# Optimization experiments

Measured on AMD Instinct MI355X. Metric: run time of the kernel, lower is better.

Reference implementation:

```python
import jax, jax.numpy as jnp
import numpy as np

N_NODES = 50000
N_EDGES = 800000
IN_CH = 96
HID = 128
OUT_CH = 2


def _glorot(key, shape):
    lim = 1.0 / np.sqrt(shape[0])
    return jax.random.uniform(key, shape, jnp.float32, -lim, lim)


def setup_inputs() -> dict:
    key = jax.random.key(0)
    ks = jax.random.split(key, 16)
    x = jax.random.normal(ks[0], (N_NODES, IN_CH), jnp.float32)
    edge_index = jax.random.randint(ks[1], (2, N_EDGES), 0, N_NODES, jnp.int64)
    dims = [(IN_CH, HID), (HID, HID), (HID, HID // 2)]
    params = {}
    for i, (di, do) in enumerate(dims, start=1):
        params[f"Wl{i}"] = _glorot(ks[2 * i], (di, do))      # neighbor (lin_l)
        params[f"Wr{i}"] = _glorot(ks[2 * i + 1], (di, do))  # root (lin_r)
        params[f"b{i}"] = jnp.zeros((do,), jnp.float32)
    params["Wc"] = _glorot(ks[10], (HID // 2, OUT_CH))
    params["bc"] = jnp.zeros((OUT_CH,), jnp.float32)
    return {"x": x, "edge_index": edge_index, **params}


def _sage_conv(x, src, dst, Wl, Wr, b):
    # scatter-mean of source-node features into destination nodes (PyG mean aggr)
    n = x.shape[0]
    agg = jax.ops.segment_sum(x[src], dst, num_segments=n)          # [N, d]
    cnt = jax.ops.segment_sum(jnp.ones((src.shape[0], 1), x.dtype), dst, num_segments=n)
    mean = agg / jnp.maximum(cnt, 1.0)
    return mean @ Wl + x @ Wr + b


def reference(x, edge_index, Wl1, Wr1, b1, Wl2, Wr2, b2, Wl3, Wr3, b3, Wc, bc):
    src, dst = edge_index[0], edge_index[1]
    h = jax.nn.relu(_sage_conv(x, src, dst, Wl1, Wr1, b1))
    h = jax.nn.relu(_sage_conv(h, src, dst, Wl2, Wr2, b2))
    h = jax.nn.relu(_sage_conv(h, src, dst, Wl3, Wr3, b3))
    return h @ Wc + bc  # [N, 2] logits (dropout is identity at inference)
```

## Files before the change

### kernel.cpp

```cpp
#include <hip/hip_runtime.h>

#define N_NODES 50000
#define N_EDGES 800000
#define SCAN_NB ((N_NODES + 255) / 256)

#define NB_E 128
#define CH (N_EDGES / NB_E)
#define RSZ 25000
#define HALF_WORDS (RSZ / 2)

#define CVT_ITEMS  (N_NODES * 96 / 4)
#define CVT_NB  ((CVT_ITEMS + 255) / 256)
#define PACK1_NB 12
#define PACK2_NB 16
#define PACK3_NB 8
#define PREP_NB (CVT_NB + PACK1_NB + PACK2_NB + PACK3_NB)

typedef __attribute__((ext_vector_type(8))) short short8;
typedef __attribute__((ext_vector_type(8))) unsigned short ushort8;
typedef __attribute__((ext_vector_type(4))) float f32x4;

__device__ __forceinline__ float bf2f(unsigned short u) {
  unsigned int x = ((unsigned int)u) << 16;
  return __builtin_bit_cast(float, x);
}
__device__ __forceinline__ unsigned short f2bf(float f) {
  unsigned int x = __builtin_bit_cast(unsigned int, f);
  unsigned int r = x + 0x7FFFu + ((x >> 16) & 1u);
  return (unsigned short)(r >> 16);
}


__device__ __forceinline__ void pack_w_section(const float* __restrict__ Wl,
                                               const float* __restrict__ Wr,
                                               ushort* __restrict__ wcat,
                                               int K, int J2, int bid) {
  int idx = bid * 256 + threadIdx.x;
  int Jcat = 2 * J2;
  int total = (K / 8) * Jcat;
  if (idx >= total) return;
  int kk8 = idx / Jcat, j = idx % Jcat;
  const float* W = (j < J2) ? Wl : Wr;
  int jj = (j < J2) ? j : j - J2;
  ushort8 v;
  #pragma unroll
  for (int i = 0; i < 8; i++) v[i] = f2bf(W[(kk8 * 8 + i) * J2 + jj]);
  *(ushort8*)(wcat + (size_t)idx * 8) = v;
}

__global__ __launch_bounds__(256) void prep_kernel(
    const float* __restrict__ x, ushort* __restrict__ xb,
    const float* __restrict__ Wl1, const float* __restrict__ Wr1, ushort* __restrict__ wcat1,
    const float* __restrict__ Wl2, const float* __restrict__ Wr2, ushort* __restrict__ wcat2,
    const float* __restrict__ Wl3, const float* __restrict__ Wr3, ushort* __restrict__ wcat3) {
  int bid = blockIdx.x;
  if (bid < CVT_NB) {
    int i = bid * 256 + threadIdx.x;
    if (i < CVT_ITEMS) {
      f32x4 v = __builtin_nontemporal_load((const f32x4*)(x + i * 4));
      ushort4 o = make_ushort4(f2bf(v.x), f2bf(v.y), f2bf(v.z), f2bf(v.w));
      *(ushort4*)(xb + i * 4) = o;
    }
    return;
  }
  bid -= CVT_NB;
  if (bid < PACK1_NB) { pack_w_section(Wl1, Wr1, wcat1, 96, 128, bid); return; }
  bid -= PACK1_NB;
  if (bid < PACK2_NB) { pack_w_section(Wl2, Wr2, wcat2, 128, 128, bid); return; }
  bid -= PACK2_NB;
  pack_w_section(Wl3, Wr3, wcat3, 128, 64, bid);
}


__global__ __launch_bounds__(256) void hist_lds(const int* __restrict__ dst,
                                                ushort* __restrict__ hist_g) {
  __shared__ unsigned hist[HALF_WORDS];
  for (int j = threadIdx.x; j < HALF_WORDS; j += 256) hist[j] = 0;
  __syncthreads();
  int b = blockIdx.x >> 1, r = blockIdx.x & 1;
  int base = b * CH;
  for (int i = threadIdx.x; i < CH; i += 256) {
    int d = __builtin_nontemporal_load(dst + base + i);
    unsigned ld = (unsigned)(d - r * RSZ);
    if (ld < RSZ) atomicAdd(&hist[ld >> 1], (ld & 1) ? 65536u : 1u);
  }
  __syncthreads();
  unsigned* outp = (unsigned*)(hist_g + (size_t)b * N_NODES + r * RSZ);
  for (int j = threadIdx.x; j < HALF_WORDS; j += 256) outp[j] = hist[j];
}

__device__ __forceinline__ int block_excl_scan_256(int v, int tid, int* tot_out) {
  __shared__ int ws[4];
  int lane = tid & 63, wid = tid >> 6;
  int incl = v;
  #pragma unroll
  for (int off = 1; off < 64; off <<= 1) {
    int t = __shfl_up(incl, off);
    if (lane >= off) incl += t;
  }
  if (lane == 63) ws[wid] = incl;
  __syncthreads();
  int woff = 0;
  #pragma unroll
  for (int w = 0; w < 4; w++) woff += (w < wid) ? ws[w] : 0;
  *tot_out = ws[0] + ws[1] + ws[2] + ws[3];
  return woff + incl - v;
}

__global__ __launch_bounds__(256) void scanA(const ushort* __restrict__ hist_g,
                                             ushort* __restrict__ cum_g,
                                             int* __restrict__ rowptr,
                                             int* __restrict__ blocksum, int n) {
  int i = blockIdx.x * 256 + threadIdx.x;
  int run = 0;
  if (i < n) {
    for (int b = 0; b < NB_E; b++) {
      size_t o = (size_t)b * N_NODES + i;
      int c = hist_g[o];
      cum_g[o] = (ushort)run;
      run += c;
    }
  }
  int tot;
  int excl = block_excl_scan_256(run, threadIdx.x, &tot);
  if (i < n) rowptr[i] = excl;
  if (threadIdx.x == 0) blocksum[blockIdx.x] = tot;
}

__global__ __launch_bounds__(256) void scanBC(const int* __restrict__ blocksum,
                                              int* __restrict__ rowptr, int n) {
  __shared__ int exls[256];
  int tid = threadIdx.x;
  int v = (tid < SCAN_NB) ? blocksum[tid] : 0;
  int tot;
  int excl = block_excl_scan_256(v, tid, &tot);
  exls[tid] = excl;
  __syncthreads();
  int myoff = exls[blockIdx.x];
  int i = blockIdx.x * 256 + tid;
  if (i < n) rowptr[i] += myoff;
  if (blockIdx.x == 0 && tid == 0) rowptr[n] = tot;
}

__global__ __launch_bounds__(256) void fill_lds(const int* __restrict__ src,
                                                const int* __restrict__ dst,
                                                const ushort* __restrict__ cum_g,
                                                const int* __restrict__ rowptr,
                                                ushort* __restrict__ csr) {
  __shared__ unsigned cur[HALF_WORDS];
  int b = blockIdx.x >> 1, r = blockIdx.x & 1;
  const unsigned* cg = (const unsigned*)(cum_g + (size_t)b * N_NODES + r * RSZ);
  for (int j = threadIdx.x; j < HALF_WORDS; j += 256) cur[j] = cg[j];
  __syncthreads();
  int base = b * CH;
  for (int i = threadIdx.x; i < CH; i += 256) {
    int d = __builtin_nontemporal_load(dst + base + i);
    int s = __builtin_nontemporal_load(src + base + i);
    unsigned ld = (unsigned)(d - r * RSZ);
    if (ld < RSZ) {
      unsigned old = atomicAdd(&cur[ld >> 1], (ld & 1) ? 65536u : 1u);
      unsigned loc = (ld & 1) ? (old >> 16) : (old & 0xffffu);
      csr[(size_t)rowptr[d] + loc] = (ushort)s;
    }
  }
}

template <int K, int J2>
__global__ __launch_bounds__(256) void gemm_mfma(
    const ushort* __restrict__ hb, const ushort* __restrict__ wcat,
    ushort* __restrict__ tl, ushort* __restrict__ tr, int n) {
  constexpr int Jcat = 2 * J2;
  constexpr int NT = Jcat / 16;
  constexpr int KS = K / 32;

  int tid = threadIdx.x;
  int wid = tid >> 6, lane = tid & 63;
  int rg = lane >> 4, lc = lane & 15;
  int row0 = blockIdx.x * 128;
  int r0 = row0 + wid * 32 + lc;
  int r1 = r0 + 16;
  long ar0 = (long)min(r0, n - 1) * K;
  long ar1 = (long)min(r1, n - 1) * K;

  f32x4 acc[2][NT];
  #pragma unroll
  for (int mt = 0; mt < 2; mt++)
    #pragma unroll
    for (int jt = 0; jt < NT; jt++) acc[mt][jt] = (f32x4){0.f, 0.f, 0.f, 0.f};

  #pragma unroll
  for (int ks = 0; ks < KS; ks++) {
    int koff = ks * 32 + rg * 8;
    short8 a0 = *(const short8*)(hb + ar0 + koff);
    short8 a1 = *(const short8*)(hb + ar1 + koff);
    int kk8 = ks * 4 + rg;
    #pragma unroll
    for (int jt = 0; jt < NT; jt++) {
      short8 bfr = *(const short8*)(wcat + ((size_t)kk8 * Jcat + jt * 16 + lc) * 8);
      acc[0][jt] = __builtin_amdgcn_mfma_f32_16x16x32_bf16(a0, bfr, acc[0][jt], 0, 0, 0);
      acc[1][jt] = __builtin_amdgcn_mfma_f32_16x16x32_bf16(a1, bfr, acc[1][jt], 0, 0, 0);
    }
  }

  #pragma unroll
  for (int mt = 0; mt < 2; mt++) {
    int rbase = wid * 32 + mt * 16 + rg * 4;
    #pragma unroll
    for (int jt = 0; jt < NT; jt++) {
      int col = jt * 16 + lc;
      ushort* outp = (col < J2) ? tl : tr;
      int cm = (col < J2) ? col : col - J2;
      #pragma unroll
      for (int r = 0; r < 4; r++) {
        int grow = row0 + rbase + r;
        if (grow < n) outp[(size_t)grow * J2 + cm] = f2bf(acc[mt][jt][r]);
      }
    }
  }
}

__global__ __launch_bounds__(256) void agg_relu128(
    const ushort* __restrict__ tl, const ushort* __restrict__ tr,
    const float* __restrict__ bias,
    const int* __restrict__ rowptr, const ushort* __restrict__ csr,
    ushort* __restrict__ hout, int n) {
  int node = blockIdx.x * 16 + (threadIdx.x >> 4);
  int lane = threadIdx.x & 15;
  if (node >= n) return;
  int lo = rowptr[node], hi = rowptr[node + 1];
  const ushort* tb = tl + lane * 8;

  float s[8];
  #pragma unroll
  for (int i = 0; i < 8; i++) s[i] = 0.f;

  int e = lo;
  for (; e + 7 < hi; e += 8) {
    ushort8 v[8];
    #pragma unroll
    for (int q = 0; q < 8; q++) v[q] = *(const ushort8*)(tb + (size_t)csr[e + q] * 128);
    #pragma unroll
    for (int q = 0; q < 8; q++)
      #pragma unroll
      for (int i = 0; i < 8; i++) s[i] += bf2f(v[q][i]);
  }
  for (; e + 1 < hi; e += 2) {
    ushort8 v0 = *(const ushort8*)(tb + (size_t)csr[e] * 128);
    ushort8 v1 = *(const ushort8*)(tb + (size_t)csr[e + 1] * 128);
    #pragma unroll
    for (int i = 0; i < 8; i++) s[i] += bf2f(v0[i]) + bf2f(v1[i]);
  }
  if (e < hi) {
    ushort8 v0 = *(const ushort8*)(tb + (size_t)csr[e] * 128);
    #pragma unroll
    for (int i = 0; i < 8; i++) s[i] += bf2f(v0[i]);
  }

  int deg = hi - lo;
  float inv = (deg > 0) ? 1.f / (float)deg : 0.f;
  ushort8 tv = *(const ushort8*)(tr + (size_t)node * 128 + lane * 8);
  float4 b0 = *(const float4*)(bias + lane * 8);
  float4 b1 = *(const float4*)(bias + lane * 8 + 4);
  float bb[8] = {b0.x, b0.y, b0.z, b0.w, b1.x, b1.y, b1.z, b1.w};
  ushort8 o;
  #pragma unroll
  for (int i = 0; i < 8; i++) {
    float v = s[i] * inv + bf2f(tv[i]) + bb[i];
    o[i] = f2bf(v > 0.f ? v : 0.f);
  }
  *(ushort8*)(hout + (size_t)node * 128 + lane * 8) = o;
}

__global__ __launch_bounds__(256) void agg_head(
    const ushort* __restrict__ tl, const ushort* __restrict__ tr,
    const float* __restrict__ bias, const float* __restrict__ Wc,
    const float* __restrict__ bc,
    const int* __restrict__ rowptr, const ushort* __restrict__ csr,
    float* __restrict__ out, int n) {
  int node = blockIdx.x * 32 + (threadIdx.x >> 3);
  int lane = threadIdx.x & 7;
  if (node >= n) return;
  int lo = rowptr[node], hi = rowptr[node + 1];
  const ushort* tb = tl + lane * 8;

  float s[8];
  #pragma unroll
  for (int i = 0; i < 8; i++) s[i] = 0.f;

  int e = lo;
  for (; e + 7 < hi; e += 8) {
    ushort8 v[8];
    #pragma unroll
    for (int q = 0; q < 8; q++) v[q] = *(const ushort8*)(tb + (size_t)csr[e + q] * 64);
    #pragma unroll
    for (int q = 0; q < 8; q++)
      #pragma unroll
      for (int i = 0; i < 8; i++) s[i] += bf2f(v[q][i]);
  }
  for (; e + 1 < hi; e += 2) {
    ushort8 v0 = *(const ushort8*)(tb + (size_t)csr[e] * 64);
    ushort8 v1 = *(const ushort8*)(tb + (size_t)csr[e + 1] * 64);
    #pragma unroll
    for (int i = 0; i < 8; i++) s[i] += bf2f(v0[i]) + bf2f(v1[i]);
  }
  if (e < hi) {
    ushort8 v0 = *(const ushort8*)(tb + (size_t)csr[e] * 64);
    #pragma unroll
    for (int i = 0; i < 8; i++) s[i] += bf2f(v0[i]);
  }

  int deg = hi - lo;
  float inv = (deg > 0) ? 1.f / (float)deg : 0.f;
  ushort8 tv = *(const ushort8*)(tr + (size_t)node * 64 + lane * 8);
  float p0 = 0.f, p1 = 0.f;
  #pragma unroll
  for (int i = 0; i < 8; i++) {
    int k = lane * 8 + i;
    float v = s[i] * inv + bf2f(tv[i]) + bias[k];
    v = v > 0.f ? v : 0.f;
    p0 += v * Wc[k * 2 + 0];
    p1 += v * Wc[k * 2 + 1];
  }
  #pragma unroll
  for (int off = 1; off < 8; off <<= 1) {
    p0 += __shfl_xor(p0, off);
    p1 += __shfl_xor(p1, off);
  }
  if (lane == 0) {
    out[(size_t)node * 2 + 0] = p0 + bc[0];
    out[(size_t)node * 2 + 1] = p1 + bc[1];
  }
}

extern "C" void kernel_launch(void* const* d_in, const int* in_sizes, int n_in,
                              void* d_out, int out_size, void* d_ws, size_t ws_size,
                              hipStream_t stream) {
  const float* x   = (const float*)d_in[0];
  const int*   ei  = (const int*)d_in[1];
  const float* Wl1 = (const float*)d_in[2];
  const float* Wr1 = (const float*)d_in[3];
  const float* b1  = (const float*)d_in[4];
  const float* Wl2 = (const float*)d_in[5];
  const float* Wr2 = (const float*)d_in[6];
  const float* b2  = (const float*)d_in[7];
  const float* Wl3 = (const float*)d_in[8];
  const float* Wr3 = (const float*)d_in[9];
  const float* b3  = (const float*)d_in[10];
  const float* Wc  = (const float*)d_in[11];
  const float* bc  = (const float*)d_in[12];
  float* out = (float*)d_out;

  const int* src = ei;
  const int* dst = ei + N_EDGES;

  char* ws = (char*)d_ws;
  size_t off = 0;
  auto alloc = [&](size_t bytes) -> void* {
    void* p = ws + off;
    off += (bytes + 255) & ~(size_t)255;
    return p;
  };
  int*    rowptr   = (int*)alloc((N_NODES + 1) * sizeof(int));
  ushort* csr      = (ushort*)alloc(N_EDGES * sizeof(ushort));
  int*    blocksum = (int*)alloc(256 * sizeof(int));
  ushort* xb       = (ushort*)alloc((size_t)N_NODES * 96 * 2);
  ushort* wcat1    = (ushort*)alloc((size_t)96 * 256 * 2);
  ushort* wcat2    = (ushort*)alloc((size_t)128 * 256 * 2);
  ushort* wcat3    = (ushort*)alloc((size_t)128 * 128 * 2);
  ushort* tl       = (ushort*)alloc((size_t)N_NODES * 128 * 2);
  ushort* tr       = (ushort*)alloc((size_t)N_NODES * 128 * 2);
  ushort* hA       = (ushort*)alloc((size_t)N_NODES * 128 * 2);
  ushort* hB       = (ushort*)alloc((size_t)N_NODES * 128 * 2);
  (void)ws_size; (void)n_in; (void)in_sizes; (void)out_size;

  ushort* hist_g = tl;
  ushort* cum_g  = tr;

  prep_kernel<<<PREP_NB, 256, 0, stream>>>(x, xb,
                                           Wl1, Wr1, wcat1,
                                           Wl2, Wr2, wcat2,
                                           Wl3, Wr3, wcat3);

  hist_lds<<<NB_E * 2, 256, 0, stream>>>(dst, hist_g);
  scanA<<<SCAN_NB, 256, 0, stream>>>(hist_g, cum_g, rowptr, blocksum, N_NODES);
  scanBC<<<SCAN_NB, 256, 0, stream>>>(blocksum, rowptr, N_NODES);
  fill_lds<<<NB_E * 2, 256, 0, stream>>>(src, dst, cum_g, rowptr, csr);

  const int gemm_grid = (N_NODES + 127) / 128;
  const int agg_grid  = (N_NODES + 15) / 16;
  const int head_grid = (N_NODES + 31) / 32;

  gemm_mfma<96, 128><<<gemm_grid, 256, 0, stream>>>(xb, wcat1, tl, tr, N_NODES);
  agg_relu128<<<agg_grid, 256, 0, stream>>>(tl, tr, b1, rowptr, csr, hA, N_NODES);
  gemm_mfma<128, 128><<<gemm_grid, 256, 0, stream>>>(hA, wcat2, tl, tr, N_NODES);
  agg_relu128<<<agg_grid, 256, 0, stream>>>(tl, tr, b2, rowptr, csr, hB, N_NODES);
  gemm_mfma<128, 64><<<gemm_grid, 256, 0, stream>>>(hB, wcat3, tl, tr, N_NODES);
  agg_head<<<head_grid, 256, 0, stream>>>(tl, tr, b3, Wc, bc, rowptr, csr, out, N_NODES);
}
```

Before: 198.7 us.

## Fuse histogram into prep kernel and CSR fill with first-layer GEMM

Merges the edge histogram pass into the prep/convert kernel and the CSR fill pass into the first GEMM launch, using block-index ranges to run independent work concurrently and cutting two launches. Histogram and cumulative buffers move to dedicated workspace so they no longer alias tl/tr, which the fused GEMM writes. NB_E is halved to 64, so each histogram block handles twice as many edges while the scan loop gets shorter. Fused blocks carry 50KB of LDS even on the GEMM/convert paths, which may reduce occupancy for those blocks.

```diff
diff --git a/kernel.cpp b/kernel.cpp
--- a/kernel.cpp
+++ b/kernel.cpp
@@ -4,17 +4,21 @@
 #define N_EDGES 800000
 #define SCAN_NB ((N_NODES + 255) / 256)
 
-#define NB_E 128
+#define NB_E 64
 #define CH (N_EDGES / NB_E)
 #define RSZ 25000
 #define HALF_WORDS (RSZ / 2)
+#define CSRB (NB_E * 2)
 
 #define CVT_ITEMS  (N_NODES * 96 / 4)
 #define CVT_NB  ((CVT_ITEMS + 255) / 256)
 #define PACK1_NB 12
 #define PACK2_NB 16
 #define PACK3_NB 8
-#define PREP_NB (CVT_NB + PACK1_NB + PACK2_NB + PACK3_NB)
+#define K1_NB (CSRB + CVT_NB + PACK1_NB + PACK2_NB + PACK3_NB)
+
+#define GEMM_NB ((N_NODES + 127) / 128)
+#define K4_NB (GEMM_NB + CSRB)
 
 typedef __attribute__((ext_vector_type(8))) short short8;
 typedef __attribute__((ext_vector_type(8))) unsigned short ushort8;
@@ -30,6 +34,59 @@
   return (unsigned short)(r >> 16);
 }
 
+template <int K, int J2>
+__device__ __forceinline__ void gemm_body(int bid,
+    const ushort* __restrict__ hb, const ushort* __restrict__ wcat,
+    ushort* __restrict__ tl, ushort* __restrict__ tr, int n) {
+  constexpr int Jcat = 2 * J2;
+  constexpr int NT = Jcat / 16;
+  constexpr int KS = K / 32;
+
+  int tid = threadIdx.x;
+  int wid = tid >> 6, lane = tid & 63;
+  int rg = lane >> 4, lc = lane & 15;
+  int row0 = bid * 128;
+  int r0 = row0 + wid * 32 + lc;
+  int r1 = r0 + 16;
+  long ar0 = (long)min(r0, n - 1) * K;
+  long ar1 = (long)min(r1, n - 1) * K;
+
+  f32x4 acc[2][NT];
+  #pragma unroll
+  for (int mt = 0; mt < 2; mt++)
+    #pragma unroll
+    for (int jt = 0; jt < NT; jt++) acc[mt][jt] = (f32x4){0.f, 0.f, 0.f, 0.f};
+
+  #pragma unroll
+  for (int ks = 0; ks < KS; ks++) {
+    int koff = ks * 32 + rg * 8;
+    short8 a0 = *(const short8*)(hb + ar0 + koff);
+    short8 a1 = *(const short8*)(hb + ar1 + koff);
+    int kk8 = ks * 4 + rg;
+    #pragma unroll
+    for (int jt = 0; jt < NT; jt++) {
+      short8 bfr = *(const short8*)(wcat + ((size_t)kk8 * Jcat + jt * 16 + lc) * 8);
+      acc[0][jt] = __builtin_amdgcn_mfma_f32_16x16x32_bf16(a0, bfr, acc[0][jt], 0, 0, 0);
+      acc[1][jt] = __builtin_amdgcn_mfma_f32_16x16x32_bf16(a1, bfr, acc[1][jt], 0, 0, 0);
+    }
+  }
+
+  #pragma unroll
+  for (int mt = 0; mt < 2; mt++) {
+    int rbase = wid * 32 + mt * 16 + rg * 4;
+    #pragma unroll
+    for (int jt = 0; jt < NT; jt++) {
+      int col = jt * 16 + lc;
+      ushort* outp = (col < J2) ? tl : tr;
+      int cm = (col < J2) ? col : col - J2;
+      #pragma unroll
+      for (int r = 0; r < 4; r++) {
+        int grow = row0 + rbase + r;
+        if (grow < n) outp[(size_t)grow * J2 + cm] = f2bf(acc[mt][jt][r]);
+      }
+    }
+  }
+}
 
 __device__ __forceinline__ void pack_w_section(const float* __restrict__ Wl,
                                                const float* __restrict__ Wr,
@@ -48,12 +105,30 @@
   *(ushort8*)(wcat + (size_t)idx * 8) = v;
 }
 
-__global__ __launch_bounds__(256) void prep_kernel(
+__global__ __launch_bounds__(256) void k1_hist_prep(
+    const int* __restrict__ dst, ushort* __restrict__ hist_g,
     const float* __restrict__ x, ushort* __restrict__ xb,
     const float* __restrict__ Wl1, const float* __restrict__ Wr1, ushort* __restrict__ wcat1,
     const float* __restrict__ Wl2, const float* __restrict__ Wr2, ushort* __restrict__ wcat2,
     const float* __restrict__ Wl3, const float* __restrict__ Wr3, ushort* __restrict__ wcat3) {
+  __shared__ unsigned hist[HALF_WORDS];
   int bid = blockIdx.x;
+  if (bid < CSRB) {
+    for (int j = threadIdx.x; j < HALF_WORDS; j += 256) hist[j] = 0;
+    __syncthreads();
+    int b = bid >> 1, r = bid & 1;
+    int base = b * CH;
+    for (int i = threadIdx.x; i < CH; i += 256) {
+      int d = __builtin_nontemporal_load(dst + base + i);
+      unsigned ld = (unsigned)(d - r * RSZ);
+      if (ld < RSZ) atomicAdd(&hist[ld >> 1], (ld & 1) ? 65536u : 1u);
+    }
+    __syncthreads();
+    unsigned* outp = (unsigned*)(hist_g + (size_t)b * N_NODES + r * RSZ);
+    for (int j = threadIdx.x; j < HALF_WORDS; j += 256) outp[j] = hist[j];
+    return;
+  }
+  bid -= CSRB;
   if (bid < CVT_NB) {
     int i = bid * 256 + threadIdx.x;
     if (i < CVT_ITEMS) {
@@ -71,23 +146,6 @@
   pack_w_section(Wl3, Wr3, wcat3, 128, 64, bid);
 }
 
-
-__global__ __launch_bounds__(256) void hist_lds(const int* __restrict__ dst,
-                                                ushort* __restrict__ hist_g) {
-  __shared__ unsigned hist[HALF_WORDS];
-  for (int j = threadIdx.x; j < HALF_WORDS; j += 256) hist[j] = 0;
-  __syncthreads();
-  int b = blockIdx.x >> 1, r = blockIdx.x & 1;
-  int base = b * CH;
-  for (int i = threadIdx.x; i < CH; i += 256) {
-    int d = __builtin_nontemporal_load(dst + base + i);
-    unsigned ld = (unsigned)(d - r * RSZ);
-    if (ld < RSZ) atomicAdd(&hist[ld >> 1], (ld & 1) ? 65536u : 1u);
-  }
-  __syncthreads();
-  unsigned* outp = (unsigned*)(hist_g + (size_t)b * N_NODES + r * RSZ);
-  for (int j = threadIdx.x; j < HALF_WORDS; j += 256) outp[j] = hist[j];
-}
 
 __device__ __forceinline__ int block_excl_scan_256(int v, int tid, int* tot_out) {
   __shared__ int ws[4];
@@ -114,6 +172,7 @@
   int i = blockIdx.x * 256 + threadIdx.x;
   int run = 0;
   if (i < n) {
+    #pragma unroll 4
     for (int b = 0; b < NB_E; b++) {
       size_t o = (size_t)b * N_NODES + i;
       int c = hist_g[o];
@@ -142,13 +201,20 @@
   if (blockIdx.x == 0 && tid == 0) rowptr[n] = tot;
 }
 
-__global__ __launch_bounds__(256) void fill_lds(const int* __restrict__ src,
-                                                const int* __restrict__ dst,
-                                                const ushort* __restrict__ cum_g,
-                                                const int* __restrict__ rowptr,
-                                                ushort* __restrict__ csr) {
+__global__ __launch_bounds__(256) void k4_gemm1_fill(
+    const ushort* __restrict__ xb, const ushort* __restrict__ wcat1,
+    ushort* __restrict__ tl, ushort* __restrict__ tr,
+    const int* __restrict__ src, const int* __restrict__ dst,
+    const ushort* __restrict__ cum_g, const int* __restrict__ rowptr,
+    ushort* __restrict__ csr, int n) {
   __shared__ unsigned cur[HALF_WORDS];
-  int b = blockIdx.x >> 1, r = blockIdx.x & 1;
+  int bid = blockIdx.x;
+  if (bid < GEMM_NB) {
+    gemm_body<96, 128>(bid, xb, wcat1, tl, tr, n);
+    return;
+  }
+  bid -= GEMM_NB;
+  int b = bid >> 1, r = bid & 1;
   const unsigned* cg = (const unsigned*)(cum_g + (size_t)b * N_NODES + r * RSZ);
   for (int j = threadIdx.x; j < HALF_WORDS; j += 256) cur[j] = cg[j];
   __syncthreads();
@@ -169,54 +235,7 @@
 __global__ __launch_bounds__(256) void gemm_mfma(
     const ushort* __restrict__ hb, const ushort* __restrict__ wcat,
     ushort* __restrict__ tl, ushort* __restrict__ tr, int n) {
-  constexpr int Jcat = 2 * J2;
-  constexpr int NT = Jcat / 16;
-  constexpr int KS = K / 32;
-
-  int tid = threadIdx.x;
-  int wid = tid >> 6, lane = tid & 63;
-  int rg = lane >> 4, lc = lane & 15;
-  int row0 = blockIdx.x * 128;
-  int r0 = row0 + wid * 32 + lc;
-  int r1 = r0 + 16;
-  long ar0 = (long)min(r0, n - 1) * K;
-  long ar1 = (long)min(r1, n - 1) * K;
-
-  f32x4 acc[2][NT];
-  #pragma unroll
-  for (int mt = 0; mt < 2; mt++)
-    #pragma unroll
-    for (int jt = 0; jt < NT; jt++) acc[mt][jt] = (f32x4){0.f, 0.f, 0.f, 0.f};
-
-  #pragma unroll
-  for (int ks = 0; ks < KS; ks++) {
-    int koff = ks * 32 + rg * 8;
-    short8 a0 = *(const short8*)(hb + ar0 + koff);
-    short8 a1 = *(const short8*)(hb + ar1 + koff);
-    int kk8 = ks * 4 + rg;
-    #pragma unroll
-    for (int jt = 0; jt < NT; jt++) {
-      short8 bfr = *(const short8*)(wcat + ((size_t)kk8 * Jcat + jt * 16 + lc) * 8);
-      acc[0][jt] = __builtin_amdgcn_mfma_f32_16x16x32_bf16(a0, bfr, acc[0][jt], 0, 0, 0);
-      acc[1][jt] = __builtin_amdgcn_mfma_f32_16x16x32_bf16(a1, bfr, acc[1][jt], 0, 0, 0);
-    }
-  }
-
-  #pragma unroll
-  for (int mt = 0; mt < 2; mt++) {
-    int rbase = wid * 32 + mt * 16 + rg * 4;
-    #pragma unroll
-    for (int jt = 0; jt < NT; jt++) {
-      int col = jt * 16 + lc;
-      ushort* outp = (col < J2) ? tl : tr;
-      int cm = (col < J2) ? col : col - J2;
-      #pragma unroll
-      for (int r = 0; r < 4; r++) {
-        int grow = row0 + rbase + r;
-        if (grow < n) outp[(size_t)grow * J2 + cm] = f2bf(acc[mt][jt][r]);
-      }
-    }
-  }
+  gemm_body<K, J2>(blockIdx.x, hb, wcat, tl, tr, n);
 }
 
 __global__ __launch_bounds__(256) void agg_relu128(
@@ -363,6 +382,8 @@
   int*    rowptr   = (int*)alloc((N_NODES + 1) * sizeof(int));
   ushort* csr      = (ushort*)alloc(N_EDGES * sizeof(ushort));
   int*    blocksum = (int*)alloc(256 * sizeof(int));
+  ushort* hist_g   = (ushort*)alloc((size_t)NB_E * N_NODES * 2);
+  ushort* cum_g    = (ushort*)alloc((size_t)NB_E * N_NODES * 2);
   ushort* xb       = (ushort*)alloc((size_t)N_NODES * 96 * 2);
   ushort* wcat1    = (ushort*)alloc((size_t)96 * 256 * 2);
   ushort* wcat2    = (ushort*)alloc((size_t)128 * 256 * 2);
@@ -373,27 +394,21 @@
   ushort* hB       = (ushort*)alloc((size_t)N_NODES * 128 * 2);
   (void)ws_size; (void)n_in; (void)in_sizes; (void)out_size;
 
-  ushort* hist_g = tl;
-  ushort* cum_g  = tr;
-
-  prep_kernel<<<PREP_NB, 256, 0, stream>>>(x, xb,
-                                           Wl1, Wr1, wcat1,
-                                           Wl2, Wr2, wcat2,
-                                           Wl3, Wr3, wcat3);
-
-  hist_lds<<<NB_E * 2, 256, 0, stream>>>(dst, hist_g);
+  k1_hist_prep<<<K1_NB, 256, 0, stream>>>(dst, hist_g, x, xb,
+                                          Wl1, Wr1, wcat1,
+                                          Wl2, Wr2, wcat2,
+                                          Wl3, Wr3, wcat3);
   scanA<<<SCAN_NB, 256, 0, stream>>>(hist_g, cum_g, rowptr, blocksum, N_NODES);
   scanBC<<<SCAN_NB, 256, 0, stream>>>(blocksum, rowptr, N_NODES);
-  fill_lds<<<NB_E * 2, 256, 0, stream>>>(src, dst, cum_g, rowptr, csr);
-
-  const int gemm_grid = (N_NODES + 127) / 128;
+  k4_gemm1_fill<<<K4_NB, 256, 0, stream>>>(xb, wcat1, tl, tr,
+                                           src, dst, cum_g, rowptr, csr, N_NODES);
+
   const int agg_grid  = (N_NODES + 15) / 16;
   const int head_grid = (N_NODES + 31) / 32;
 
-  gemm_mfma<96, 128><<<gemm_grid, 256, 0, stream>>>(xb, wcat1, tl, tr, N_NODES);
   agg_relu128<<<agg_grid, 256, 0, stream>>>(tl, tr, b1, rowptr, csr, hA, N_NODES);
-  gemm_mfma<128, 128><<<gemm_grid, 256, 0, stream>>>(hA, wcat2, tl, tr, N_NODES);
+  gemm_mfma<128, 128><<<GEMM_NB, 256, 0, stream>>>(hA, wcat2, tl, tr, N_NODES);
   agg_relu128<<<agg_grid, 256, 0, stream>>>(tl, tr, b2, rowptr, csr, hB, N_NODES);
-  gemm_mfma<128, 64><<<gemm_grid, 256, 0, stream>>>(hB, wcat3, tl, tr, N_NODES);
+  gemm_mfma<128, 64><<<GEMM_NB, 256, 0, stream>>>(hB, wcat3, tl, tr, N_NODES);
   agg_head<<<head_grid, 256, 0, stream>>>(tl, tr, b3, Wc, bc, rowptr, csr, out, N_NODES);
 }
```

After: 215.4 us. 8.4% more time.
